# Kernel optimization log

Hardware: AMD Instinct MI355X
Metric: run time of the kernel (lower is better)

## Reference

```python
import jax, jax.numpy as jnp
import numpy as np

NEG_SLOPE = 0.2
HEADS = 4
C = 64            # hidden_channels
NUM_CLASSES = 12
NUM_GRAPHS = 512


def gatv2_conv(x, src, dst, Wl, Wr, att, bias, heads, out_ch, num_nodes):
    """PyG GATv2Conv: gather -> LeakyReLU attention -> segment softmax -> scatter.
    x: [N, Fin]; src/dst: [E]; Wl/Wr: [Fin, heads*out_ch]; att: [heads, out_ch]; bias: [heads*out_ch].
    Messages flow src -> dst; heads are concatenated."""
    xl = (x @ Wl).reshape(num_nodes, heads, out_ch)  # source-side transform
    xr = (x @ Wr).reshape(num_nodes, heads, out_ch)  # target-side transform
    e = jax.nn.leaky_relu(xl[src] + xr[dst], NEG_SLOPE)      # [E, H, C]
    score = jnp.einsum('ehc,hc->eh', e, att)                  # [E, H]
    smax = jax.ops.segment_max(score, dst, num_segments=num_nodes)  # [N, H]
    ex = jnp.exp(score - smax[dst])
    denom = jax.ops.segment_sum(ex, dst, num_segments=num_nodes)    # [N, H]
    alpha = ex / (denom[dst] + 1e-16)                         # [E, H]
    out = jax.ops.segment_sum(alpha[:, :, None] * xl[src], dst, num_segments=num_nodes)
    return out.reshape(num_nodes, heads * out_ch) + bias


def add_self_loops(edge_index, num_nodes):
    loop = jnp.arange(num_nodes, dtype=edge_index.dtype)
    src = jnp.concatenate([edge_index[0], loop])
    dst = jnp.concatenate([edge_index[1], loop])
    return src, dst


def setup_inputs() -> dict:
    key = jax.random.key(0)
    ks = jax.random.split(key, 20)
    N, F, E = 50000, 128, 800000

    def w(k, shape):
        return (jax.random.normal(k, shape) * 0.1).astype(jnp.float32)

    inp = {
        'x': jax.random.normal(ks[0], (N, F), dtype=jnp.float32),
        'edge_index': jax.random.randint(ks[1], (2, E), 0, N),
        'batch': jnp.sort(jax.random.randint(ks[2], (N,), 0, NUM_GRAPHS)),
        # conv1: (-1,-1) lazy -> Fin=F, heads=4
        'W1l': w(ks[3], (F, HEADS * C)), 'W1r': w(ks[4], (F, HEADS * C)),
        'a1': w(ks[5], (HEADS, C)), 'b1': jnp.zeros((HEADS * C,), jnp.float32),
        # conv2: Fin = hidden*heads = 256, heads=4
        'W2l': w(ks[6], (HEADS * C, HEADS * C)), 'W2r': w(ks[7], (HEADS * C, HEADS * C)),
        'a2': w(ks[8], (HEADS, C)), 'b2': jnp.zeros((HEADS * C,), jnp.float32),
        # conv3: Fin = 256, heads=1
        'W3l': w(ks[9], (HEADS * C, C)), 'W3r': w(ks[10], (HEADS * C, C)),
        'a3': w(ks[11], (1, C)), 'b3': jnp.zeros((C,), jnp.float32),
        # MLP head (lazy Linear(-1, ...) resolves to C after conv3 heads=1)
        'lin1_w': w(ks[12], (C, C)), 'lin1_b': jnp.zeros((C,), jnp.float32),
        'lin2_w': w(ks[13], (C, C)), 'lin2_b': jnp.zeros((C,), jnp.float32),
        'lin3_w': w(ks[14], (C, NUM_CLASSES)), 'lin3_b': jnp.zeros((NUM_CLASSES,), jnp.float32),
    }
    return inp


def reference(x, edge_index, batch,
              W1l, W1r, a1, b1,
              W2l, W2r, a2, b2,
              W3l, W3r, a3, b3,
              lin1_w, lin1_b, lin2_w, lin2_b, lin3_w, lin3_b):
    N = x.shape[0]
    src0, dst0 = edge_index[0], edge_index[1]          # conv1: add_self_loops=False
    src1, dst1 = add_self_loops(edge_index, N)         # conv2/3: add_self_loops=True

    h = gatv2_conv(x, src0, dst0, W1l, W1r, a1, b1, HEADS, C, N)
    h = jax.nn.relu(h)
    h = gatv2_conv(h, src1, dst1, W2l, W2r, a2, b2, HEADS, C, N)
    h = jax.nn.relu(h)
    h = gatv2_conv(h, src1, dst1, W3l, W3r, a3, b3, 1, C, N)

    # global mean pool over graphs
    s = jax.ops.segment_sum(h, batch, num_segments=NUM_GRAPHS)
    cnt = jax.ops.segment_sum(jnp.ones((N, 1), h.dtype), batch, num_segments=NUM_GRAPHS)
    g = s / jnp.maximum(cnt, 1.0)

    g = jax.nn.relu(g @ lin1_w + lin1_b)
    # dropout p=0.5 is identity in eval mode
    g = jax.nn.relu(g @ lin2_w + lin2_b)
    return jax.nn.softmax(g @ lin3_w + lin3_b, axis=1)
```

## Files before the change

kernel.cpp:

```cpp
#include <hip/hip_runtime.h>
#include <hip/hip_bf16.h>
#include <cstdint>
#include <cstddef>

typedef short bf16x8 __attribute__((ext_vector_type(8)));
typedef float f32x4 __attribute__((ext_vector_type(4)));
typedef float f32x2 __attribute__((ext_vector_type(2)));
typedef unsigned short u16x4v __attribute__((ext_vector_type(4)));

__device__ __forceinline__ float bf2f(unsigned short u) {
  union { unsigned int u; float f; } v; v.u = ((unsigned int)u) << 16; return v.f;
}
__device__ __forceinline__ unsigned short f2bf(float f) {
  union { float f; unsigned int u; } v; v.f = f;
  unsigned int r = v.u + 0x7fffu + ((v.u >> 16) & 1u);
  return (unsigned short)(r >> 16);
}
__device__ __forceinline__ int pack2(float a, float b) {
  return (int)f2bf(a) | ((int)f2bf(b) << 16);
}
__device__ __forceinline__ float bcf(unsigned int u) {
  union { unsigned int u; float f; } v; v.u = u; return v.f;
}
__device__ __forceinline__ f32x2 bf2x2(unsigned int u) {
  f32x2 r;
  r.x = bcf(u << 16);
  r.y = bcf(u & 0xffff0000u);
  return r;
}
__device__ __forceinline__ void gll16(const void* g, void* l) {
  __builtin_amdgcn_global_load_lds(
      (const __attribute__((address_space(1))) unsigned int*)g,
      (__attribute__((address_space(3))) unsigned int*)l, 16, 0, 0);
}
template<int CTRL>
__device__ __forceinline__ float dpp_ror_add(float p) {
  int t = __builtin_amdgcn_update_dpp(0, __builtin_bit_cast(int, p), CTRL, 0xf, 0xf, true);
  return p + __builtin_bit_cast(float, t);
}
__device__ __forceinline__ float row16_sum(float p) {
  p = dpp_ror_add<0x121>(p);
  p = dpp_ror_add<0x122>(p);
  p = dpp_ror_add<0x124>(p);
  p = dpp_ror_add<0x128>(p);
  return p;
}

#define LOG2E 1.44269504088896f
#define THR2  11.5415603271f

struct WPack {
  const float* in[6];
  unsigned short* out[6];
  int K[6], Ncol[6];
  int start[7];
};
__global__ __launch_bounds__(256) void convert_all(WPack p) {
  int idx = blockIdx.x * 256 + threadIdx.x;
  #pragma unroll
  for (int s = 0; s < 6; ++s) {
    if (idx >= p.start[s] && idx < p.start[s + 1]) {
      int lidx = idx - p.start[s];
      int k = lidx / p.Ncol[s], n = lidx % p.Ncol[s];
      p.out[s][n * p.K[s] + k] = f2bf(p.in[s][lidx]);
    }
  }
}

template<int BN, int WAVES_M, int WAVES_N, bool AF32, bool GLL>
__global__ __launch_bounds__(256) void gemm_dual(
    const void* __restrict__ Av,
    const unsigned short* __restrict__ BtL, const unsigned short* __restrict__ BtR,
    unsigned short* __restrict__ outL, unsigned short* __restrict__ outR,
    int M, int K, int Ncol) {
  constexpr int BM = 128, BK = 64;
  constexpr int WTM = BM / WAVES_M, WTN = BN / WAVES_N;
  constexpr int MR = WTM / 16, NR = WTN / 16;
  const unsigned short* __restrict__ Bt = blockIdx.z ? BtR : BtL;
  unsigned short* __restrict__ outp = blockIdx.z ? outR : outL;

  __shared__ alignas(16) unsigned short lAt[BM * BK];
  __shared__ alignas(16) unsigned short lBt[BN * BK];

  int t = threadIdx.x;
  int lane = t & 63, wid = t >> 6;
  int wm = wid / WAVES_N, wn = wid % WAVES_N;
  int rowBase = blockIdx.x * BM;
  int colBase = blockIdx.y * BN;

  f32x4 acc[MR][NR] = {};

  for (int k0 = 0; k0 < K; k0 += BK) {
    if constexpr (GLL) {
      const unsigned short* A = (const unsigned short*)Av;
      #pragma unroll
      for (int p = 0; p < BM / 32; ++p) {
        int chunk = wid * (BM / 32) + p;
        int row = chunk * 8 + (lane >> 3);
        int c = (lane & 7) ^ (row & 7);
        gll16(A + (size_t)(rowBase + row) * K + k0 + c * 8, &lAt[chunk * 512]);
      }
      #pragma unroll
      for (int p = 0; p < BN / 32; ++p) {
        int chunk = wid * (BN / 32) + p;
        int row = chunk * 8 + (lane >> 3);
        int c = (lane & 7) ^ (row & 7);
        gll16(Bt + (size_t)(colBase + row) * K + k0 + c * 8, &lBt[chunk * 512]);
      }
    } else {
      #pragma unroll
      for (int p = 0; p < (BM * 8) / 256; ++p) {
        int lin = p * 256 + t;
        int row = lin >> 3, c = lin & 7;
        int gr = rowBase + row;
        int4 w = make_int4(0, 0, 0, 0);
        if constexpr (AF32) {
          const float* A = (const float*)Av;
          if (gr < M) {
            const float* ap = A + (size_t)gr * K + k0 + c * 8;
            f32x4 f0 = *reinterpret_cast<const f32x4*>(ap);
            f32x4 f1 = *reinterpret_cast<const f32x4*>(ap + 4);
            w.x = pack2(f0[0], f0[1]); w.y = pack2(f0[2], f0[3]);
            w.z = pack2(f1[0], f1[1]); w.w = pack2(f1[2], f1[3]);
          }
        } else {
          const unsigned short* A = (const unsigned short*)Av;
          if (gr < M) w = *reinterpret_cast<const int4*>(A + (size_t)gr * K + k0 + c * 8);
        }
        *reinterpret_cast<int4*>(&lAt[row * 64 + ((c ^ (row & 7)) * 8)]) = w;
      }
      #pragma unroll
      for (int p = 0; p < (BN * 8) / 256; ++p) {
        int lin = p * 256 + t;
        int row = lin >> 3, c = lin & 7;
        int4 v = *reinterpret_cast<const int4*>(Bt + (size_t)(colBase + row) * K + k0 + c * 8);
        *reinterpret_cast<int4*>(&lBt[row * 64 + ((c ^ (row & 7)) * 8)]) = v;
      }
    }
    __syncthreads();
    #pragma unroll
    for (int kk = 0; kk < 2; ++kk) {
      bf16x8 af[MR], bfr[NR];
      int cidx = kk * 4 + (lane >> 4);
      #pragma unroll
      for (int mi = 0; mi < MR; ++mi) {
        int row = wm * WTM + mi * 16 + (lane & 15);
        af[mi] = *reinterpret_cast<const bf16x8*>(&lAt[row * 64 + ((cidx ^ (row & 7)) * 8)]);
      }
      #pragma unroll
      for (int ni = 0; ni < NR; ++ni) {
        int row = wn * WTN + ni * 16 + (lane & 15);
        bfr[ni] = *reinterpret_cast<const bf16x8*>(&lBt[row * 64 + ((cidx ^ (row & 7)) * 8)]);
      }
      #pragma unroll
      for (int mi = 0; mi < MR; ++mi)
        #pragma unroll
        for (int ni = 0; ni < NR; ++ni)
          acc[mi][ni] = __builtin_amdgcn_mfma_f32_16x16x32_bf16(af[mi], bfr[ni], acc[mi][ni], 0, 0, 0);
    }
    __syncthreads();
  }
  #pragma unroll
  for (int mi = 0; mi < MR; ++mi)
    #pragma unroll
    for (int ni = 0; ni < NR; ++ni) {
      int col = colBase + wn * WTN + ni * 16 + (lane & 15);
      #pragma unroll
      for (int r = 0; r < 4; ++r) {
        int row = rowBase + wm * WTM + mi * 16 + (lane >> 4) * 4 + r;
        if (row < M) outp[(size_t)row * Ncol + col] = f2bf(acc[mi][ni][r]);
      }
    }
}

__global__ __launch_bounds__(256) void hist_kernel(const int* __restrict__ dst, int* __restrict__ counts, int E) {
  int e = blockIdx.x * 256 + threadIdx.x;
  if (e < E) atomicAdd(&counts[dst[e]], 1);
}

__global__ __launch_bounds__(256) void scan_block_deg(
    const int* __restrict__ in, int* __restrict__ out, int* __restrict__ sums,
    int* __restrict__ binTotal, int* __restrict__ blockBase, int n) {
  __shared__ int lh[256];
  __shared__ int wsum[4];
  lh[threadIdx.x] = 0;
  __syncthreads();
  int i = blockIdx.x * 256 + threadIdx.x;
  int lane = threadIdx.x & 63, wid = threadIdx.x >> 6;
  int v = (i < n) ? in[i] : 0;
  if (i < n) atomicAdd(&lh[v < 255 ? v : 255], 1);
  int s = v;
  #pragma unroll
  for (int d = 1; d < 64; d <<= 1) { int tt = __shfl_up(s, d); if (lane >= d) s += tt; }
  if (lane == 63) wsum[wid] = s;
  __syncthreads();
  int off = 0;
  for (int w = 0; w < wid; ++w) off += wsum[w];
  if (i < n) out[i] = off + s - v;
  if (threadIdx.x == 255) sums[blockIdx.x] = off + s;
  int c = lh[threadIdx.x];
  blockBase[blockIdx.x * 256 + threadIdx.x] = c ? atomicAdd(&binTotal[threadIdx.x], c) : 0;
}

__global__ __launch_bounds__(256) void scan2_offsets(
    const int* __restrict__ bsums, int* __restrict__ boffs,
    const int* __restrict__ binTotal, int* __restrict__ binStart, int n) {
  __shared__ int ws[4];
  int t = threadIdx.x;
  int lane = t & 63, w = t >> 6;
  {
    int v = (t < n) ? bsums[t] : 0;
    int s = v;
    #pragma unroll
    for (int d = 1; d < 64; d <<= 1) { int tt = __shfl_up(s, d); if (lane >= d) s += tt; }
    if (lane == 63) ws[w] = s;
    __syncthreads();
    int off = 0;
    for (int u = 0; u < w; ++u) off += ws[u];
    if (t < n) boffs[t] = off + s - v;
    __syncthreads();
  }
  {
    int v = binTotal[255 - t];
    int s = v;
    #pragma unroll
    for (int d = 1; d < 64; d <<= 1) { int tt = __shfl_up(s, d); if (lane >= d) s += tt; }
    if (lane == 63) ws[w] = s;
    __syncthreads();
    int off = 0;
    for (int u = 0; u < w; ++u) off += ws[u];
    binStart[255 - t] = off + s - v;
  }
}

__global__ __launch_bounds__(256) void scan_add_place(
    int* __restrict__ rs, const int* __restrict__ boffs, int* __restrict__ cursor,
    const int* __restrict__ counts, const int* __restrict__ binStart,
    const int* __restrict__ blockBase, int* __restrict__ perm, int n, int E) {
  __shared__ int lcur[256];
  lcur[threadIdx.x] = binStart[threadIdx.x] + blockBase[blockIdx.x * 256 + threadIdx.x];
  __syncthreads();
  int i = blockIdx.x * 256 + threadIdx.x;
  if (i < n) {
    int v = rs[i] + boffs[blockIdx.x];
    rs[i] = v;
    cursor[i] = v;
    int d = counts[i]; if (d > 255) d = 255;
    perm[atomicAdd(&lcur[d], 1)] = i;
  }
  if (i == 0) rs[n] = E;
}

__global__ __launch_bounds__(256) void scatter_kernel(const int* __restrict__ src, const int* __restrict__ dst,
                                                      int* __restrict__ cursor, int* __restrict__ csr, int E) {
  int e = blockIdx.x * 256 + threadIdx.x;
  if (e < E) {
    int p = atomicAdd(&cursor[dst[e]], 1);
    csr[p] = src[e];
  }
}

template<int VEC2>
__device__ __forceinline__ void load_row2(const unsigned short* __restrict__ base,
                                          int s, int lane, f32x2* v) {
  uint2 uv = *reinterpret_cast<const uint2*>(base + (size_t)s * 256 + lane * 4);
  v[0] = bf2x2(uv.x);
  v[1] = bf2x2(uv.y);
}

template<int VEC2>
__device__ __forceinline__ float edge_score2(const f32x2* xv, const f32x2* xrv, const f32x2* attv) {
  f32x2 p2 = {0.f, 0.f};
  #pragma unroll
  for (int j = 0; j < VEC2; ++j) {
    f32x2 tv = xv[j] + xrv[j];
    f32x2 sl = 0.2f * tv;
    tv.x = fmaxf(tv.x, sl.x); tv.y = fmaxf(tv.y, sl.y);
    p2.x = fmaf(tv.x, attv[j].x, p2.x);
    p2.y = fmaf(tv.y, attv[j].y, p2.y);
  }
  return row16_sum(p2.x + p2.y);
}

template<bool SELF, bool RELU>
__global__ __launch_bounds__(256) void edge_agg4(
    const unsigned short* __restrict__ xl, const unsigned short* __restrict__ xr,
    const float* __restrict__ att, const float* __restrict__ bias,
    const int* __restrict__ rowstart, const int* __restrict__ csr,
    const int* __restrict__ perm,
    unsigned short* __restrict__ out, int N) {
  int wave = threadIdx.x >> 6, lane = threadIdx.x & 63;
  int gid = blockIdx.x * 4 + wave;
  if (gid >= N) return;
  int node = perm[gid];

  f32x2 attv[2];
  {
    f32x4 a4 = *reinterpret_cast<const f32x4*>(att + lane * 4);
    attv[0].x = a4[0] * LOG2E; attv[0].y = a4[1] * LOG2E;
    attv[1].x = a4[2] * LOG2E; attv[1].y = a4[3] * LOG2E;
  }
  f32x2 xrv[2];
  load_row2<2>(xr, node, lane, xrv);

  int s0 = rowstart[node], s1 = rowstart[node + 1];
  int end = s1 + (SELF ? 1 : 0);

  float m = 0.f, l = 0.f;
  f32x2 acc[2] = {{0.f, 0.f}, {0.f, 0.f}};

  int i = s0;
  if (i < end) {
    int s = (i < s1) ? csr[i] : node;
    f32x2 xv[2];
    load_row2<2>(xl, s, lane, xv);
    m = edge_score2<2>(xv, xrv, attv);
    l = 1.f;
    acc[0] = xv[0]; acc[1] = xv[1];
    ++i;
  }
  for (; i + 4 <= end; i += 4) {
    int s_[4];
    f32x2 x_[4][2];
    float p_[4], w_[4];
    #pragma unroll
    for (int q = 0; q < 4; ++q) s_[q] = (i + q < s1) ? csr[i + q] : node;
    #pragma unroll
    for (int q = 0; q < 4; ++q) load_row2<2>(xl, s_[q], lane, x_[q]);
    #pragma unroll
    for (int q = 0; q < 4; ++q) p_[q] = edge_score2<2>(x_[q], xrv, attv);
    float mx = fmaxf(fmaxf(p_[0], p_[1]), fmaxf(p_[2], p_[3]));
    if (__any(mx > m + THR2)) {
      float mn = fmaxf(m, mx);
      float sc = __builtin_amdgcn_exp2f(m - mn);
      l *= sc;
      acc[0] *= sc; acc[1] *= sc;
      m = mn;
    }
    #pragma unroll
    for (int q = 0; q < 4; ++q) w_[q] = __builtin_amdgcn_exp2f(p_[q] - m);
    l += (w_[0] + w_[1]) + (w_[2] + w_[3]);
    #pragma unroll
    for (int j = 0; j < 2; ++j) {
      f32x2 a = acc[j];
      a.x = fmaf(w_[0], x_[0][j].x, a.x); a.y = fmaf(w_[0], x_[0][j].y, a.y);
      a.x = fmaf(w_[1], x_[1][j].x, a.x); a.y = fmaf(w_[1], x_[1][j].y, a.y);
      a.x = fmaf(w_[2], x_[2][j].x, a.x); a.y = fmaf(w_[2], x_[2][j].y, a.y);
      a.x = fmaf(w_[3], x_[3][j].x, a.x); a.y = fmaf(w_[3], x_[3][j].y, a.y);
      acc[j] = a;
    }
  }
  for (; i < end; ++i) {
    int s = (i < s1) ? csr[i] : node;
    f32x2 xv[2];
    load_row2<2>(xl, s, lane, xv);
    float p = edge_score2<2>(xv, xrv, attv);
    if (__any(p > m + THR2)) {
      float mn = fmaxf(m, p);
      float sc = __builtin_amdgcn_exp2f(m - mn);
      l *= sc;
      acc[0] *= sc; acc[1] *= sc;
      m = mn;
    }
    float w = __builtin_amdgcn_exp2f(p - m);
    l += w;
    #pragma unroll
    for (int j = 0; j < 2; ++j) {
      acc[j].x = fmaf(w, xv[j].x, acc[j].x);
      acc[j].y = fmaf(w, xv[j].y, acc[j].y);
    }
  }

  float rec = 1.f / (l + 1e-16f);
  f32x4 b4 = *reinterpret_cast<const f32x4*>(bias + lane * 4);
  u16x4v w4;
  float o0 = fmaf(acc[0].x, rec, b4[0]);
  float o1 = fmaf(acc[0].y, rec, b4[1]);
  float o2 = fmaf(acc[1].x, rec, b4[2]);
  float o3 = fmaf(acc[1].y, rec, b4[3]);
  if (RELU) {
    o0 = fmaxf(o0, 0.f); o1 = fmaxf(o1, 0.f);
    o2 = fmaxf(o2, 0.f); o3 = fmaxf(o3, 0.f);
  }
  w4[0] = f2bf(o0); w4[1] = f2bf(o1); w4[2] = f2bf(o2); w4[3] = f2bf(o3);
  *reinterpret_cast<u16x4v*>(out + (size_t)node * 256 + lane * 4) = w4;
}

template<bool SELF, bool RELU>
__global__ __launch_bounds__(256) void edge_agg1(
    const unsigned short* __restrict__ xl, const unsigned short* __restrict__ xr,
    const float* __restrict__ att, const float* __restrict__ bias,
    const int* __restrict__ rowstart, const int* __restrict__ csr,
    const int* __restrict__ perm,
    unsigned short* __restrict__ out, int N) {
  int wave = threadIdx.x >> 6, lane = threadIdx.x & 63;
  int gid = blockIdx.x * 4 + wave;
  if (gid >= N) return;
  int node = perm[gid];

  float attv = att[lane] * LOG2E;
  float xrv = bf2f(xr[(size_t)node * 64 + lane]);

  int s0 = rowstart[node], s1 = rowstart[node + 1];
  int end = s1 + (SELF ? 1 : 0);

  float m = 0.f, l = 0.f, acc = 0.f;

  auto score = [&](float xv) {
    float tv = xv + xrv;
    tv = fmaxf(tv, 0.2f * tv);
    float p = row16_sum(tv * attv);
    p += __shfl_xor(p, 16);
    p += __shfl_xor(p, 32);
    return p;
  };

  int i = s0;
  if (i < end) {
    int s = (i < s1) ? csr[i] : node;
    float xv = bf2f(xl[(size_t)s * 64 + lane]);
    m = score(xv);
    l = 1.f;
    acc = xv;
    ++i;
  }
  for (; i + 4 <= end; i += 4) {
    int s_[4];
    float x_[4], p_[4], w_[4];
    #pragma unroll
    for (int q = 0; q < 4; ++q) s_[q] = (i + q < s1) ? csr[i + q] : node;
    #pragma unroll
    for (int q = 0; q < 4; ++q) x_[q] = bf2f(xl[(size_t)s_[q] * 64 + lane]);
    #pragma unroll
    for (int q = 0; q < 4; ++q) p_[q] = score(x_[q]);
    float mx = fmaxf(fmaxf(p_[0], p_[1]), fmaxf(p_[2], p_[3]));
    if (__any(mx > m + THR2)) {
      float mn = fmaxf(m, mx);
      float sc = __builtin_amdgcn_exp2f(m - mn);
      l *= sc; acc *= sc; m = mn;
    }
    #pragma unroll
    for (int q = 0; q < 4; ++q) w_[q] = __builtin_amdgcn_exp2f(p_[q] - m);
    l += (w_[0] + w_[1]) + (w_[2] + w_[3]);
    acc = fmaf(w_[0], x_[0], fmaf(w_[1], x_[1], fmaf(w_[2], x_[2], fmaf(w_[3], x_[3], acc))));
  }
  for (; i < end; ++i) {
    int s = (i < s1) ? csr[i] : node;
    float xv = bf2f(xl[(size_t)s * 64 + lane]);
    float p = score(xv);
    if (__any(p > m + THR2)) {
      float mn = fmaxf(m, p);
      float sc = __builtin_amdgcn_exp2f(m - mn);
      l *= sc; acc *= sc; m = mn;
    }
    float w = __builtin_amdgcn_exp2f(p - m);
    l += w;
    acc = fmaf(w, xv, acc);
  }

  float rec = 1.f / (l + 1e-16f);
  float o = fmaf(acc, rec, bias[lane]);
  if (RELU) o = fmaxf(o, 0.f);
  out[(size_t)node * 64 + lane] = f2bf(o);
}

__global__ __launch_bounds__(256) void pool_mlp(
    const unsigned short* __restrict__ h, const int* __restrict__ batch,
    const float* __restrict__ w1, const float* __restrict__ b1,
    const float* __restrict__ w2, const float* __restrict__ b2,
    const float* __restrict__ w3, const float* __restrict__ b3,
    float* __restrict__ out, int N) {
  int g = blockIdx.x;
  int lo = 0, hi = N;
  while (lo < hi) { int mid = (lo + hi) >> 1; if (batch[mid] < g) lo = mid + 1; else hi = mid; }
  int n0 = lo;
  hi = N;
  while (lo < hi) { int mid = (lo + hi) >> 1; if (batch[mid] < g + 1) lo = mid + 1; else hi = mid; }
  int n1 = lo;

  int t = threadIdx.x;
  int c2 = t & 31, r = t >> 5;
  float ax = 0.f, ay = 0.f;
  for (int n = n0 + r; n < n1; n += 8) {
    unsigned int u = *reinterpret_cast<const unsigned int*>(h + (size_t)n * 64 + c2 * 2);
    ax += bf2f((unsigned short)(u & 0xffffu));
    ay += bf2f((unsigned short)(u >> 16));
  }
  __shared__ float redx[8][32], redy[8][32];
  __shared__ float sh[64];
  redx[r][c2] = ax; redy[r][c2] = ay;
  __syncthreads();
  if (t < 64) {
    int lane = t;
    float s = 0.f;
    #pragma unroll
    for (int q = 0; q < 8; ++q) s += (lane & 1) ? redy[q][lane >> 1] : redx[q][lane >> 1];
    float cnt = fmaxf((float)(n1 - n0), 1.f);
    sh[lane] = s / cnt;
    float h1 = b1[lane];
    for (int k = 0; k < 64; ++k) h1 = fmaf(sh[k], w1[k * 64 + lane], h1);
    h1 = fmaxf(h1, 0.f);
    sh[lane] = h1;
    float h2 = b2[lane];
    for (int k = 0; k < 64; ++k) h2 = fmaf(sh[k], w2[k * 64 + lane], h2);
    h2 = fmaxf(h2, 0.f);
    sh[lane] = h2;
    float lg = -INFINITY;
    if (lane < 12) {
      lg = b3[lane];
      for (int k = 0; k < 64; ++k) lg = fmaf(sh[k], w3[k * 12 + lane], lg);
    }
    float mx = lg;
    #pragma unroll
    for (int msk = 1; msk < 64; msk <<= 1) mx = fmaxf(mx, __shfl_xor(mx, msk));
    float ex = (lane < 12) ? __expf(lg - mx) : 0.f;
    float sm = ex;
    #pragma unroll
    for (int msk = 1; msk < 64; msk <<= 1) sm += __shfl_xor(sm, msk);
    if (lane < 12) out[(size_t)g * 12 + lane] = ex / sm;
  }
}

extern "C" void kernel_launch(void* const* d_in, const int* in_sizes, int n_in,
                              void* d_out, int out_size, void* d_ws, size_t ws_size,
                              hipStream_t stream) {
  const float* x    = (const float*)d_in[0];
  const int* edge   = (const int*)d_in[1];
  const int* batch  = (const int*)d_in[2];
  const float* W1l  = (const float*)d_in[3];
  const float* W1r  = (const float*)d_in[4];
  const float* a1   = (const float*)d_in[5];
  const float* b1   = (const float*)d_in[6];
  const float* W2l  = (const float*)d_in[7];
  const float* W2r  = (const float*)d_in[8];
  const float* a2   = (const float*)d_in[9];
  const float* b2   = (const float*)d_in[10];
  const float* W3l  = (const float*)d_in[11];
  const float* W3r  = (const float*)d_in[12];
  const float* a3   = (const float*)d_in[13];
  const float* b3   = (const float*)d_in[14];
  const float* lw1  = (const float*)d_in[15];
  const float* lb1  = (const float*)d_in[16];
  const float* lw2  = (const float*)d_in[17];
  const float* lb2  = (const float*)d_in[18];
  const float* lw3  = (const float*)d_in[19];
  const float* lb3  = (const float*)d_in[20];

  const int E = in_sizes[1] / 2;
  const int N = in_sizes[2];
  const int F0 = in_sizes[0] / N;
  const int G = out_size / 12;
  const int* src = edge;
  const int* dst = edge + E;

  const int gx = (N + 127) / 128;
  const int Mpad = gx * 128;
  const int nb = (N + 255) / 256;

  char* p = (char*)d_ws;
  auto alloc = [&](size_t bytes) { char* q = p; p += (bytes + 255) & ~(size_t)255; return q; };
  unsigned short* bufA = (unsigned short*)alloc((size_t)Mpad * 256 * 2);
  unsigned short* bufB = (unsigned short*)alloc((size_t)Mpad * 256 * 2);
  unsigned short* bufH = (unsigned short*)alloc((size_t)Mpad * 256 * 2);
  unsigned short* Wt1L = (unsigned short*)alloc(128 * 256 * 2);
  unsigned short* Wt1R = (unsigned short*)alloc(128 * 256 * 2);
  unsigned short* Wt2L = (unsigned short*)alloc(256 * 256 * 2);
  unsigned short* Wt2R = (unsigned short*)alloc(256 * 256 * 2);
  unsigned short* Wt3L = (unsigned short*)alloc(256 * 64 * 2);
  unsigned short* Wt3R = (unsigned short*)alloc(256 * 64 * 2);
  int* counts    = (int*)alloc((size_t)N * 4);
  int* binTotal  = (int*)alloc(256 * 4);
  int* binStart  = (int*)alloc(256 * 4);
  int* blockBase = (int*)alloc((size_t)nb * 256 * 4);
  int* rowstart  = (int*)alloc((size_t)(N + 1) * 4);
  int* cursor    = (int*)alloc((size_t)N * 4);
  int* perm      = (int*)alloc((size_t)N * 4);
  int* bsums     = (int*)alloc(4096 * 4);
  int* boffs     = (int*)alloc(4096 * 4);
  int* csr       = (int*)alloc((size_t)E * 4);

  size_t countsPad = ((size_t)N * 4 + 255) & ~(size_t)255;
  hipMemsetAsync(counts, 0, countsPad + 256 * 4, stream);
  hist_kernel<<<(E + 255) / 256, 256, 0, stream>>>(dst, counts, E);
  scan_block_deg<<<nb, 256, 0, stream>>>(counts, rowstart, bsums, binTotal, blockBase, N);
  scan2_offsets<<<1, 256, 0, stream>>>(bsums, boffs, binTotal, binStart, nb);
  scan_add_place<<<nb, 256, 0, stream>>>(rowstart, boffs, cursor, counts, binStart, blockBase, perm, N, E);
  scatter_kernel<<<(E + 255) / 256, 256, 0, stream>>>(src, dst, cursor, csr, E);

  {
    WPack wp;
    const float* ins[6] = {W1l, W1r, W2l, W2r, W3l, W3r};
    unsigned short* outs[6] = {Wt1L, Wt1R, Wt2L, Wt2R, Wt3L, Wt3R};
    int Ks[6] = {F0, F0, 256, 256, 256, 256};
    int Ns[6] = {256, 256, 256, 256, 64, 64};
    int acc0 = 0;
    for (int s = 0; s < 6; ++s) {
      wp.in[s] = ins[s]; wp.out[s] = outs[s]; wp.K[s] = Ks[s]; wp.Ncol[s] = Ns[s];
      wp.start[s] = acc0; acc0 += Ks[s] * Ns[s];
    }
    wp.start[6] = acc0;
    convert_all<<<(acc0 + 255) / 256, 256, 0, stream>>>(wp);
  }

  int ne = (N + 3) / 4;

  gemm_dual<128, 2, 2, true, false><<<dim3(gx, 2, 2), 256, 0, stream>>>(x, Wt1L, Wt1R, bufA, bufB, N, F0, 256);
  edge_agg4<false, true><<<ne, 256, 0, stream>>>(bufA, bufB, a1, b1, rowstart, csr, perm, bufH, N);

  gemm_dual<128, 2, 2, false, true><<<dim3(gx, 2, 2), 256, 0, stream>>>(bufH, Wt2L, Wt2R, bufA, bufB, N, 256, 256);
  edge_agg4<true, true><<<ne, 256, 0, stream>>>(bufA, bufB, a2, b2, rowstart, csr, perm, bufH, N);

  gemm_dual<64, 4, 1, false, true><<<dim3(gx, 1, 2), 256, 0, stream>>>(bufH, Wt3L, Wt3R, bufA, bufB, N, 256, 64);
  edge_agg1<true, false><<<ne, 256, 0, stream>>>(bufA, bufB, a3, b3, rowstart, csr, perm, bufH, N);

  pool_mlp<<<G, 256, 0, stream>>>(bufH, batch, lw1, lb1, lw2, lb2, lw3, lb3,
                                  (float*)d_out, N);
}
```

Before: 467.4 us.

## Pre-convert x to bf16, unify GEMM loads, deepen edge aggregation unrolling

Adds a separate kernel that converts x to bf16 so every GEMM can load its A tiles with direct global-to-LDS loads, and removes the fp32 register-staging path. The edge aggregation kernels move the self-loop and first-edge handling out of the main loop and drop the per-edge self-loop select. Their main loops now process 6 (4-head) or 8 (1-head) neighbours per iteration instead of 4, to keep more gathers in flight. This costs an extra pass over x, more register pressure, and a longer remainder loop for low-degree nodes.

```diff
diff --git a/kernel.cpp b/kernel.cpp
--- a/kernel.cpp
+++ b/kernel.cpp
@@ -5,7 +5,6 @@
 
 typedef short bf16x8 __attribute__((ext_vector_type(8)));
 typedef float f32x4 __attribute__((ext_vector_type(4)));
-typedef float f32x2 __attribute__((ext_vector_type(2)));
 typedef unsigned short u16x4v __attribute__((ext_vector_type(4)));
 
 __device__ __forceinline__ float bf2f(unsigned short u) {
@@ -15,18 +14,6 @@
   union { float f; unsigned int u; } v; v.f = f;
   unsigned int r = v.u + 0x7fffu + ((v.u >> 16) & 1u);
   return (unsigned short)(r >> 16);
-}
-__device__ __forceinline__ int pack2(float a, float b) {
-  return (int)f2bf(a) | ((int)f2bf(b) << 16);
-}
-__device__ __forceinline__ float bcf(unsigned int u) {
-  union { unsigned int u; float f; } v; v.u = u; return v.f;
-}
-__device__ __forceinline__ f32x2 bf2x2(unsigned int u) {
-  f32x2 r;
-  r.x = bcf(u << 16);
-  r.y = bcf(u & 0xffff0000u);
-  return r;
 }
 __device__ __forceinline__ void gll16(const void* g, void* l) {
   __builtin_amdgcn_global_load_lds(
@@ -67,9 +54,21 @@
   }
 }
 
-template<int BN, int WAVES_M, int WAVES_N, bool AF32, bool GLL>
+__global__ __launch_bounds__(256) void convert_x(const float* __restrict__ in,
+                                                 unsigned short* __restrict__ out, int n4) {
+  int i = blockIdx.x * 256 + threadIdx.x;
+  if (i < n4) {
+    f32x4 v = *reinterpret_cast<const f32x4*>(in + (size_t)i * 4);
+    u16x4v o;
+    #pragma unroll
+    for (int j = 0; j < 4; ++j) o[j] = f2bf(v[j]);
+    *reinterpret_cast<u16x4v*>(out + (size_t)i * 4) = o;
+  }
+}
+
+template<int BN, int WAVES_M, int WAVES_N>
 __global__ __launch_bounds__(256) void gemm_dual(
-    const void* __restrict__ Av,
+    const unsigned short* __restrict__ A,
     const unsigned short* __restrict__ BtL, const unsigned short* __restrict__ BtR,
     unsigned short* __restrict__ outL, unsigned short* __restrict__ outR,
     int M, int K, int Ncol) {
@@ -91,51 +90,19 @@
   f32x4 acc[MR][NR] = {};
 
   for (int k0 = 0; k0 < K; k0 += BK) {
-    if constexpr (GLL) {
-      const unsigned short* A = (const unsigned short*)Av;
-      #pragma unroll
-      for (int p = 0; p < BM / 32; ++p) {
-        int chunk = wid * (BM / 32) + p;
-        int row = chunk * 8 + (lane >> 3);
-        int c = (lane & 7) ^ (row & 7);
-        gll16(A + (size_t)(rowBase + row) * K + k0 + c * 8, &lAt[chunk * 512]);
-      }
-      #pragma unroll
-      for (int p = 0; p < BN / 32; ++p) {
-        int chunk = wid * (BN / 32) + p;
-        int row = chunk * 8 + (lane >> 3);
-        int c = (lane & 7) ^ (row & 7);
-        gll16(Bt + (size_t)(colBase + row) * K + k0 + c * 8, &lBt[chunk * 512]);
-      }
-    } else {
-      #pragma unroll
-      for (int p = 0; p < (BM * 8) / 256; ++p) {
-        int lin = p * 256 + t;
-        int row = lin >> 3, c = lin & 7;
-        int gr = rowBase + row;
-        int4 w = make_int4(0, 0, 0, 0);
-        if constexpr (AF32) {
-          const float* A = (const float*)Av;
-          if (gr < M) {
-            const float* ap = A + (size_t)gr * K + k0 + c * 8;
-            f32x4 f0 = *reinterpret_cast<const f32x4*>(ap);
-            f32x4 f1 = *reinterpret_cast<const f32x4*>(ap + 4);
-            w.x = pack2(f0[0], f0[1]); w.y = pack2(f0[2], f0[3]);
-            w.z = pack2(f1[0], f1[1]); w.w = pack2(f1[2], f1[3]);
-          }
-        } else {
-          const unsigned short* A = (const unsigned short*)Av;
-          if (gr < M) w = *reinterpret_cast<const int4*>(A + (size_t)gr * K + k0 + c * 8);
-        }
-        *reinterpret_cast<int4*>(&lAt[row * 64 + ((c ^ (row & 7)) * 8)]) = w;
-      }
-      #pragma unroll
-      for (int p = 0; p < (BN * 8) / 256; ++p) {
-        int lin = p * 256 + t;
-        int row = lin >> 3, c = lin & 7;
-        int4 v = *reinterpret_cast<const int4*>(Bt + (size_t)(colBase + row) * K + k0 + c * 8);
-        *reinterpret_cast<int4*>(&lBt[row * 64 + ((c ^ (row & 7)) * 8)]) = v;
-      }
+    #pragma unroll
+    for (int p = 0; p < BM / 32; ++p) {
+      int chunk = wid * (BM / 32) + p;
+      int row = chunk * 8 + (lane >> 3);
+      int c = (lane & 7) ^ (row & 7);
+      gll16(A + (size_t)(rowBase + row) * K + k0 + c * 8, &lAt[chunk * 512]);
+    }
+    #pragma unroll
+    for (int p = 0; p < BN / 32; ++p) {
+      int chunk = wid * (BN / 32) + p;
+      int row = chunk * 8 + (lane >> 3);
+      int c = (lane & 7) ^ (row & 7);
+      gll16(Bt + (size_t)(colBase + row) * K + k0 + c * 8, &lBt[chunk * 512]);
     }
     __syncthreads();
     #pragma unroll
@@ -260,28 +227,6 @@
   }
 }
 
-template<int VEC2>
-__device__ __forceinline__ void load_row2(const unsigned short* __restrict__ base,
-                                          int s, int lane, f32x2* v) {
-  uint2 uv = *reinterpret_cast<const uint2*>(base + (size_t)s * 256 + lane * 4);
-  v[0] = bf2x2(uv.x);
-  v[1] = bf2x2(uv.y);
-}
-
-template<int VEC2>
-__device__ __forceinline__ float edge_score2(const f32x2* xv, const f32x2* xrv, const f32x2* attv) {
-  f32x2 p2 = {0.f, 0.f};
-  #pragma unroll
-  for (int j = 0; j < VEC2; ++j) {
-    f32x2 tv = xv[j] + xrv[j];
-    f32x2 sl = 0.2f * tv;
-    tv.x = fmaxf(tv.x, sl.x); tv.y = fmaxf(tv.y, sl.y);
-    p2.x = fmaf(tv.x, attv[j].x, p2.x);
-    p2.y = fmaf(tv.y, attv[j].y, p2.y);
-  }
-  return row16_sum(p2.x + p2.y);
-}
-
 template<bool SELF, bool RELU>
 __global__ __launch_bounds__(256) void edge_agg4(
     const unsigned short* __restrict__ xl, const unsigned short* __restrict__ xr,
@@ -294,95 +239,122 @@
   if (gid >= N) return;
   int node = perm[gid];
 
-  f32x2 attv[2];
+  float attv[4];
   {
     f32x4 a4 = *reinterpret_cast<const f32x4*>(att + lane * 4);
-    attv[0].x = a4[0] * LOG2E; attv[0].y = a4[1] * LOG2E;
-    attv[1].x = a4[2] * LOG2E; attv[1].y = a4[3] * LOG2E;
-  }
-  f32x2 xrv[2];
-  load_row2<2>(xr, node, lane, xrv);
+    #pragma unroll
+    for (int j = 0; j < 4; ++j) attv[j] = a4[j] * LOG2E;
+  }
+  float xrv[4];
+  {
+    u16x4v r4 = *reinterpret_cast<const u16x4v*>(xr + (size_t)node * 256 + lane * 4);
+    #pragma unroll
+    for (int j = 0; j < 4; ++j) xrv[j] = bf2f(r4[j]);
+  }
 
   int s0 = rowstart[node], s1 = rowstart[node + 1];
-  int end = s1 + (SELF ? 1 : 0);
-
-  float m = 0.f, l = 0.f;
-  f32x2 acc[2] = {{0.f, 0.f}, {0.f, 0.f}};
+
+  auto score4 = [&](u16x4v raw, float* xv) -> float {
+    float p = 0.f;
+    #pragma unroll
+    for (int j = 0; j < 4; ++j) {
+      xv[j] = bf2f(raw[j]);
+      float tv = xv[j] + xrv[j];
+      tv = fmaxf(tv, 0.2f * tv);
+      p = fmaf(tv, attv[j], p);
+    }
+    return row16_sum(p);
+  };
+
+  float m, l;
+  float acc[4];
+
+  if constexpr (SELF) {
+    u16x4v raw = *reinterpret_cast<const u16x4v*>(xl + (size_t)node * 256 + lane * 4);
+    float xv[4];
+    m = score4(raw, xv);
+    l = 1.f;
+    #pragma unroll
+    for (int j = 0; j < 4; ++j) acc[j] = xv[j];
+  } else {
+    if (s0 >= s1) {
+      u16x4v w4;
+      f32x4 b4 = *reinterpret_cast<const f32x4*>(bias + lane * 4);
+      #pragma unroll
+      for (int j = 0; j < 4; ++j) {
+        float o = b4[j];
+        if (RELU) o = fmaxf(o, 0.f);
+        w4[j] = f2bf(o);
+      }
+      *reinterpret_cast<u16x4v*>(out + (size_t)node * 256 + lane * 4) = w4;
+      return;
+    }
+    u16x4v raw = *reinterpret_cast<const u16x4v*>(xl + (size_t)csr[s0] * 256 + lane * 4);
+    float xv[4];
+    m = score4(raw, xv);
+    l = 1.f;
+    #pragma unroll
+    for (int j = 0; j < 4; ++j) acc[j] = xv[j];
+    ++s0;
+  }
 
   int i = s0;
-  if (i < end) {
-    int s = (i < s1) ? csr[i] : node;
-    f32x2 xv[2];
-    load_row2<2>(xl, s, lane, xv);
-    m = edge_score2<2>(xv, xrv, attv);
-    l = 1.f;
-    acc[0] = xv[0]; acc[1] = xv[1];
-    ++i;
-  }
-  for (; i + 4 <= end; i += 4) {
-    int s_[4];
-    f32x2 x_[4][2];
-    float p_[4], w_[4];
-    #pragma unroll
-    for (int q = 0; q < 4; ++q) s_[q] = (i + q < s1) ? csr[i + q] : node;
-    #pragma unroll
-    for (int q = 0; q < 4; ++q) load_row2<2>(xl, s_[q], lane, x_[q]);
-    #pragma unroll
-    for (int q = 0; q < 4; ++q) p_[q] = edge_score2<2>(x_[q], xrv, attv);
-    float mx = fmaxf(fmaxf(p_[0], p_[1]), fmaxf(p_[2], p_[3]));
+  for (; i + 6 <= s1; i += 6) {
+    u16x4v raw[6];
+    #pragma unroll
+    for (int q = 0; q < 6; ++q)
+      raw[q] = *reinterpret_cast<const u16x4v*>(xl + (size_t)csr[i + q] * 256 + lane * 4);
+    float xv[6][4], p_[6];
+    #pragma unroll
+    for (int q = 0; q < 6; ++q) p_[q] = score4(raw[q], xv[q]);
+    float mx = fmaxf(fmaxf(fmaxf(p_[0], p_[1]), fmaxf(p_[2], p_[3])), fmaxf(p_[4], p_[5]));
     if (__any(mx > m + THR2)) {
       float mn = fmaxf(m, mx);
       float sc = __builtin_amdgcn_exp2f(m - mn);
       l *= sc;
-      acc[0] *= sc; acc[1] *= sc;
+      #pragma unroll
+      for (int j = 0; j < 4; ++j) acc[j] *= sc;
       m = mn;
     }
-    #pragma unroll
-    for (int q = 0; q < 4; ++q) w_[q] = __builtin_amdgcn_exp2f(p_[q] - m);
-    l += (w_[0] + w_[1]) + (w_[2] + w_[3]);
-    #pragma unroll
-    for (int j = 0; j < 2; ++j) {
-      f32x2 a = acc[j];
-      a.x = fmaf(w_[0], x_[0][j].x, a.x); a.y = fmaf(w_[0], x_[0][j].y, a.y);
-      a.x = fmaf(w_[1], x_[1][j].x, a.x); a.y = fmaf(w_[1], x_[1][j].y, a.y);
-      a.x = fmaf(w_[2], x_[2][j].x, a.x); a.y = fmaf(w_[2], x_[2][j].y, a.y);
-      a.x = fmaf(w_[3], x_[3][j].x, a.x); a.y = fmaf(w_[3], x_[3][j].y, a.y);
+    float w_[6];
+    #pragma unroll
+    for (int q = 0; q < 6; ++q) w_[q] = __builtin_amdgcn_exp2f(p_[q] - m);
+    l += ((w_[0] + w_[1]) + (w_[2] + w_[3])) + (w_[4] + w_[5]);
+    #pragma unroll
+    for (int j = 0; j < 4; ++j) {
+      float a = acc[j];
+      #pragma unroll
+      for (int q = 0; q < 6; ++q) a = fmaf(w_[q], xv[q][j], a);
       acc[j] = a;
     }
   }
-  for (; i < end; ++i) {
-    int s = (i < s1) ? csr[i] : node;
-    f32x2 xv[2];
-    load_row2<2>(xl, s, lane, xv);
-    float p = edge_score2<2>(xv, xrv, attv);
+  for (; i < s1; ++i) {
+    u16x4v raw = *reinterpret_cast<const u16x4v*>(xl + (size_t)csr[i] * 256 + lane * 4);
+    float xv[4];
+    float p = score4(raw, xv);
     if (__any(p > m + THR2)) {
       float mn = fmaxf(m, p);
       float sc = __builtin_amdgcn_exp2f(m - mn);
       l *= sc;
-      acc[0] *= sc; acc[1] *= sc;
+      #pragma unroll
+      for (int j = 0; j < 4; ++j) acc[j] *= sc;
       m = mn;
     }
     float w = __builtin_amdgcn_exp2f(p - m);
     l += w;
     #pragma unroll
-    for (int j = 0; j < 2; ++j) {
-      acc[j].x = fmaf(w, xv[j].x, acc[j].x);
-      acc[j].y = fmaf(w, xv[j].y, acc[j].y);
-    }
+    for (int j = 0; j < 4; ++j) acc[j] = fmaf(w, xv[j], acc[j]);
   }
 
   float rec = 1.f / (l + 1e-16f);
   f32x4 b4 = *reinterpret_cast<const f32x4*>(bias + lane * 4);
   u16x4v w4;
-  float o0 = fmaf(acc[0].x, rec, b4[0]);
-  float o1 = fmaf(acc[0].y, rec, b4[1]);
-  float o2 = fmaf(acc[1].x, rec, b4[2]);
-  float o3 = fmaf(acc[1].y, rec, b4[3]);
-  if (RELU) {
-    o0 = fmaxf(o0, 0.f); o1 = fmaxf(o1, 0.f);
-    o2 = fmaxf(o2, 0.f); o3 = fmaxf(o3, 0.f);
-  }
-  w4[0] = f2bf(o0); w4[1] = f2bf(o1); w4[2] = f2bf(o2); w4[3] = f2bf(o3);
+  #pragma unroll
+  for (int j = 0; j < 4; ++j) {
+    float o = fmaf(acc[j], rec, b4[j]);
+    if (RELU) o = fmaxf(o, 0.f);
+    w4[j] = f2bf(o);
+  }
   *reinterpret_cast<u16x4v*>(out + (size_t)node * 256 + lane * 4) = w4;
 }
 
@@ -402,9 +374,6 @@
   float xrv = bf2f(xr[(size_t)node * 64 + lane]);
 
   int s0 = rowstart[node], s1 = rowstart[node + 1];
-  int end = s1 + (SELF ? 1 : 0);
-
-  float m = 0.f, l = 0.f, acc = 0.f;
 
   auto score = [&](float xv) {
     float tv = xv + xrv;
@@ -415,38 +384,46 @@
     return p;
   };
 
+  float m, l, acc;
+  if constexpr (SELF) {
+    float xv = bf2f(xl[(size_t)node * 64 + lane]);
+    m = score(xv); l = 1.f; acc = xv;
+  } else {
+    if (s0 >= s1) {
+      float o = bias[lane];
+      if (RELU) o = fmaxf(o, 0.f);
+      out[(size_t)node * 64 + lane] = f2bf(o);
+      return;
+    }
+    float xv = bf2f(xl[(size_t)csr[s0] * 64 + lane]);
+    m = score(xv); l = 1.f; acc = xv;
+    ++s0;
+  }
+
   int i = s0;
-  if (i < end) {
-    int s = (i < s1) ? csr[i] : node;
-    float xv = bf2f(xl[(size_t)s * 64 + lane]);
-    m = score(xv);
-    l = 1.f;
-    acc = xv;
-    ++i;
-  }
-  for (; i + 4 <= end; i += 4) {
-    int s_[4];
-    float x_[4], p_[4], w_[4];
-    #pragma unroll
-    for (int q = 0; q < 4; ++q) s_[q] = (i + q < s1) ? csr[i + q] : node;
-    #pragma unroll
-    for (int q = 0; q < 4; ++q) x_[q] = bf2f(xl[(size_t)s_[q] * 64 + lane]);
-    #pragma unroll
-    for (int q = 0; q < 4; ++q) p_[q] = score(x_[q]);
-    float mx = fmaxf(fmaxf(p_[0], p_[1]), fmaxf(p_[2], p_[3]));
+  for (; i + 8 <= s1; i += 8) {
+    float x_[8], p_[8], w_[8];
+    #pragma unroll
+    for (int q = 0; q < 8; ++q) x_[q] = bf2f(xl[(size_t)csr[i + q] * 64 + lane]);
+    #pragma unroll
+    for (int q = 0; q < 8; ++q) p_[q] = score(x_[q]);
+    float mx = fmaxf(fmaxf(fmaxf(p_[0], p_[1]), fmaxf(p_[2], p_[3])),
+                     fmaxf(fmaxf(p_[4], p_[5]), fmaxf(p_[6], p_[7])));
     if (__any(mx > m + THR2)) {
       float mn = fmaxf(m, mx);
       float sc = __builtin_amdgcn_exp2f(m - mn);
       l *= sc; acc *= sc; m = mn;
     }
     #pragma unroll
-    for (int q = 0; q < 4; ++q) w_[q] = __builtin_amdgcn_exp2f(p_[q] - m);
-    l += (w_[0] + w_[1]) + (w_[2] + w_[3]);
-    acc = fmaf(w_[0], x_[0], fmaf(w_[1], x_[1], fmaf(w_[2], x_[2], fmaf(w_[3], x_[3], acc))));
-  }
-  for (; i < end; ++i) {
-    int s = (i < s1) ? csr[i] : node;
-    float xv = bf2f(xl[(size_t)s * 64 + lane]);
+    for (int q = 0; q < 8; ++q) w_[q] = __builtin_amdgcn_exp2f(p_[q] - m);
+    l += ((w_[0] + w_[1]) + (w_[2] + w_[3])) + ((w_[4] + w_[5]) + (w_[6] + w_[7]));
+    float a = acc;
+    #pragma unroll
+    for (int q = 0; q < 8; ++q) a = fmaf(w_[q], x_[q], a);
+    acc = a;
+  }
+  for (; i < s1; ++i) {
+    float xv = bf2f(xl[(size_t)csr[i] * 64 + lane]);
     float p = score(xv);
     if (__any(p > m + THR2)) {
       float mn = fmaxf(m, p);
@@ -562,6 +539,7 @@
   unsigned short* bufA = (unsigned short*)alloc((size_t)Mpad * 256 * 2);
   unsigned short* bufB = (unsigned short*)alloc((size_t)Mpad * 256 * 2);
   unsigned short* bufH = (unsigned short*)alloc((size_t)Mpad * 256 * 2);
+  unsigned short* xbf  = (unsigned short*)alloc((size_t)Mpad * 128 * 2);
   unsigned short* Wt1L = (unsigned short*)alloc(128 * 256 * 2);
   unsigned short* Wt1R = (unsigned short*)alloc(128 * 256 * 2);
   unsigned short* Wt2L = (unsigned short*)alloc(256 * 256 * 2);
@@ -601,16 +579,20 @@
     wp.start[6] = acc0;
     convert_all<<<(acc0 + 255) / 256, 256, 0, stream>>>(wp);
   }
+  {
+    int n4 = (N * F0) / 4;
+    convert_x<<<(n4 + 255) / 256, 256, 0, stream>>>(x, xbf, n4);
+  }
 
   int ne = (N + 3) / 4;
 
-  gemm_dual<128, 2, 2, true, false><<<dim3(gx, 2, 2), 256, 0, stream>>>(x, Wt1L, Wt1R, bufA, bufB, N, F0, 256);
+  gemm_dual<128, 2, 2><<<dim3(gx, 2, 2), 256, 0, stream>>>(xbf, Wt1L, Wt1R, bufA, bufB, N, F0, 256);
   edge_agg4<false, true><<<ne, 256, 0, stream>>>(bufA, bufB, a1, b1, rowstart, csr, perm, bufH, N);
 
-  gemm_dual<128, 2, 2, false, true><<<dim3(gx, 2, 2), 256, 0, stream>>>(bufH, Wt2L, Wt2R, bufA, bufB, N, 256, 256);
+  gemm_dual<128, 2, 2><<<dim3(gx, 2, 2), 256, 0, stream>>>(bufH, Wt2L, Wt2R, bufA, bufB, N, 256, 256);
   edge_agg4<true, true><<<ne, 256, 0, stream>>>(bufA, bufB, a2, b2, rowstart, csr, perm, bufH, N);
 
-  gemm_dual<64, 4, 1, false, true><<<dim3(gx, 1, 2), 256, 0, stream>>>(bufH, Wt3L, Wt3R, bufA, bufB, N, 256, 64);
+  gemm_dual<64, 4, 1><<<dim3(gx, 1, 2), 256, 0, stream>>>(bufH, Wt3L, Wt3R, bufA, bufB, N, 256, 64);
   edge_agg1<true, false><<<ne, 256, 0, stream>>>(bufA, bufB, a3, b3, rowstart, csr, perm, bufH, N);
 
   pool_mlp<<<G, 256, 0, stream>>>(bufH, batch, lw1, lb1, lw2, lb2, lw3, lb3,
```

Measured after the change: 480.2 us. 1.03x slower.
